# Optimization experiments

Measured on AMD Instinct MI355X. Metric: run time of the kernel, lower is better.

The kernel has to match this reference:

```python
import jax, jax.numpy as jnp
import numpy as np

WINDOW = 64
STRIDE = 4
IMG_H = 512
IMG_W = 512


def _extract_windows(img, W, stride):
    # img: [H, Wd] -> windows [oh*ow, W, W] (row-major over the output grid,
    # matching torch F.unfold ordering)
    H, Wd = img.shape
    oh = (H - W) // stride + 1
    ow = (Wd - W) // stride + 1
    rows = (jnp.arange(oh) * stride)[:, None] + jnp.arange(W)[None, :]   # [oh, W]
    cols = (jnp.arange(ow) * stride)[:, None] + jnp.arange(W)[None, :]   # [ow, W]
    windows = img[rows[:, None, :, None], cols[None, :, None, :]]        # [oh, ow, W, W]
    return windows.reshape(oh * ow, W, W), oh, ow


def setup_inputs() -> dict:
    key = jax.random.key(0)
    X = jax.random.uniform(key, (1, 1, IMG_H, IMG_W), dtype=jnp.float32)
    return {"X": X}


def reference(X):
    W = WINDOW
    stride = STRIDE
    img = X[0, 0]
    windows, oh, ow = _extract_windows(img, W, stride)  # [N, W, W]

    # sizes = 2**arange(log2(W), 1, -1): e.g. W=64 -> [64, 32, 16, 8, 4]
    sizes = (2 ** np.arange(int(np.log2(W)), 1, -1)).astype(np.int64)
    log_sizes = jnp.log(jnp.asarray(sizes, dtype=jnp.float32))  # [S]

    log_db = []
    for s in sizes:
        s = int(s)
        # box partition of each window: [N, W//s, s, W//s, s]
        r = windows.reshape(-1, W // s, s, W // s, s)
        smax = r.max(axis=(2, 4))
        smin = r.min(axis=(2, 4))
        d_b = (smax - smin).sum(axis=(1, 2))  # [N] per-window box-count sum
        log_db.append(jnp.log(d_b))
    log_db = jnp.stack(log_db)  # [S, N]

    # lstsq with a single column (no intercept): slope = <x, y> / <x, x>
    slope = (log_sizes @ log_db) / (log_sizes @ log_sizes)  # [N]
    fd = -slope
    return fd.reshape(1, 1, oh, ow)
```

## Files before the change

### kernel.cpp

```cpp
#include <hip/hip_runtime.h>
#include <math.h>

#define IMG_W 512
#define OW 113
#define N_WIN (113 * 113)
#define LSTRIDE 128

#define OFF4  0
#define OFF8  16384
#define OFF16 32768
#define OFF32 49152
#define OFF64 65536

__device__ __forceinline__ float max4f(float4 v) { return fmaxf(fmaxf(v.x, v.y), fmaxf(v.z, v.w)); }
__device__ __forceinline__ float min4f(float4 v) { return fminf(fminf(v.x, v.y), fminf(v.z, v.w)); }

__global__ __launch_bounds__(256) void fd_pyramid(const float* __restrict__ X,
                                                  float* __restrict__ ws) {
    float* diff4  = ws + OFF4;
    float* diff8  = ws + OFF8;
    float* diff16 = ws + OFF16;
    float* diff32 = ws + OFF32;
    float* diff64 = ws + OFF64;

    const int bi = blockIdx.x >> 4;
    const int bj = blockIdx.x & 15;
    const int r0 = bi * 8, c0 = bj * 8;
    const int t = threadIdx.x;

    __shared__ float tmax[23][24], tmin[23][24];
    __shared__ float p8x[22][24],  p8n[22][24];
    __shared__ float p16x[20][24], p16n[20][24];
    __shared__ float p32x[16][24], p32n[16][24];

    for (int idx = t; idx < 23 * 23; idx += 256) {
        const int lr = idx / 23, lc = idx - lr * 23;
        const int gr = min(r0 + lr, 127);
        const int gc = min(c0 + lc, 127);
        const float* p = X + (gr * 4) * IMG_W + gc * 4;
        float4 a = *(const float4*)(p);
        float4 b = *(const float4*)(p + IMG_W);
        float4 c = *(const float4*)(p + 2 * IMG_W);
        float4 d = *(const float4*)(p + 3 * IMG_W);
        tmax[lr][lc] = fmaxf(fmaxf(max4f(a), max4f(b)), fmaxf(max4f(c), max4f(d)));
        tmin[lr][lc] = fminf(fminf(min4f(a), min4f(b)), fminf(min4f(c), min4f(d)));
    }
    __syncthreads();

    for (int idx = t; idx < 22 * 22; idx += 256) {
        const int lr = idx / 22, lc = idx - lr * 22;
        float x = fmaxf(fmaxf(tmax[lr][lc],     tmax[lr][lc + 1]),
                        fmaxf(tmax[lr + 1][lc], tmax[lr + 1][lc + 1]));
        float n = fminf(fminf(tmin[lr][lc],     tmin[lr][lc + 1]),
                        fminf(tmin[lr + 1][lc], tmin[lr + 1][lc + 1]));
        p8x[lr][lc] = x;
        p8n[lr][lc] = n;
        if (lr < 8 && lc < 8) {
            diff4[(r0 + lr) * LSTRIDE + c0 + lc] = tmax[lr][lc] - tmin[lr][lc];
            diff8[(r0 + lr) * LSTRIDE + c0 + lc] = x - n;
        }
    }
    __syncthreads();

    for (int idx = t; idx < 20 * 20; idx += 256) {
        const int lr = idx / 20, lc = idx - lr * 20;
        float x = fmaxf(fmaxf(p8x[lr][lc],     p8x[lr][lc + 2]),
                        fmaxf(p8x[lr + 2][lc], p8x[lr + 2][lc + 2]));
        float n = fminf(fminf(p8n[lr][lc],     p8n[lr][lc + 2]),
                        fminf(p8n[lr + 2][lc], p8n[lr + 2][lc + 2]));
        p16x[lr][lc] = x;
        p16n[lr][lc] = n;
        if (lr < 8 && lc < 8)
            diff16[(r0 + lr) * LSTRIDE + c0 + lc] = x - n;
    }
    __syncthreads();

    for (int idx = t; idx < 16 * 16; idx += 256) {
        const int lr = idx >> 4, lc = idx & 15;
        float x = fmaxf(fmaxf(p16x[lr][lc],     p16x[lr][lc + 4]),
                        fmaxf(p16x[lr + 4][lc], p16x[lr + 4][lc + 4]));
        float n = fminf(fminf(p16n[lr][lc],     p16n[lr][lc + 4]),
                        fminf(p16n[lr + 4][lc], p16n[lr + 4][lc + 4]));
        p32x[lr][lc] = x;
        p32n[lr][lc] = n;
        if (lr < 8 && lc < 8)
            diff32[(r0 + lr) * LSTRIDE + c0 + lc] = x - n;
    }
    __syncthreads();

    if (t < 64) {
        const int lr = t >> 3, lc = t & 7;
        float x = fmaxf(fmaxf(p32x[lr][lc],     p32x[lr][lc + 8]),
                        fmaxf(p32x[lr + 8][lc], p32x[lr + 8][lc + 8]));
        float n = fminf(fminf(p32n[lr][lc],     p32n[lr][lc + 8]),
                        fminf(p32n[lr + 8][lc], p32n[lr + 8][lc + 8]));
        diff64[(r0 + lr) * LSTRIDE + c0 + lc] = x - n;
    }
}

__global__ __launch_bounds__(256) void fd_final(const float* __restrict__ ws,
                                                float* __restrict__ out) {
    const int w = blockIdx.x * 256 + threadIdx.x;
    if (w >= N_WIN) return;
    const int ti = w / OW;
    const int tj = w - ti * OW;

    const float* diff4  = ws + OFF4;
    const float* diff8  = ws + OFF8;
    const float* diff16 = ws + OFF16;
    const float* diff32 = ws + OFF32;
    const float* diff64 = ws + OFF64;

    float d4 = 0.f;
    #pragma unroll
    for (int a = 0; a < 16; ++a) {
        const float* row = diff4 + (ti + a) * LSTRIDE + tj;
        #pragma unroll
        for (int b = 0; b < 16; ++b) d4 += row[b];
    }
    float d8 = 0.f;
    #pragma unroll
    for (int a = 0; a < 8; ++a) {
        const float* row = diff8 + (ti + 2 * a) * LSTRIDE + tj;
        #pragma unroll
        for (int b = 0; b < 8; ++b) d8 += row[2 * b];
    }
    float d16 = 0.f;
    #pragma unroll
    for (int a = 0; a < 4; ++a) {
        const float* row = diff16 + (ti + 4 * a) * LSTRIDE + tj;
        #pragma unroll
        for (int b = 0; b < 4; ++b) d16 += row[4 * b];
    }
    float d32 = 0.f;
    #pragma unroll
    for (int a = 0; a < 2; ++a) {
        const float* row = diff32 + (ti + 8 * a) * LSTRIDE + tj;
        #pragma unroll
        for (int b = 0; b < 2; ++b) d32 += row[8 * b];
    }
    const float d64 = diff64[ti * LSTRIDE + tj];

    const float LN2 = 0.69314718055994530942f;
    const float num = 6.f * logf(d64) + 5.f * logf(d32) + 4.f * logf(d16)
                    + 3.f * logf(d8)  + 2.f * logf(d4);
    out[w] = -num / (90.0f * LN2);
}

extern "C" void kernel_launch(void* const* d_in, const int* in_sizes, int n_in,
                              void* d_out, int out_size, void* d_ws, size_t ws_size,
                              hipStream_t stream) {
    const float* X = (const float*)d_in[0];
    float* out = (float*)d_out;
    float* ws = (float*)d_ws;
    fd_pyramid<<<256, 256, 0, stream>>>(X, ws);
    fd_final<<<(N_WIN + 255) / 256, 256, 0, stream>>>(ws, out);
}
```

Measured before the change: 61.23 us.

## Fuse pyramid and window-sum kernels into one block-local kernel

Merges the two kernels into one. Each block keeps its per-level max-min differences in shared memory and sums the windows of an 8x8 output tile directly, with four threads per window combined by wavefront shuffles. This removes the global workspace round trip and the second launch. In exchange each block holds more shared memory, and fewer blocks are launched (225 instead of 256).

```diff
diff --git a/kernel.cpp b/kernel.cpp
--- a/kernel.cpp
+++ b/kernel.cpp
@@ -3,47 +3,37 @@
 
 #define IMG_W 512
 #define OW 113
-#define N_WIN (113 * 113)
-#define LSTRIDE 128
-
-#define OFF4  0
-#define OFF8  16384
-#define OFF16 32768
-#define OFF32 49152
-#define OFF64 65536
+#define DS 27
 
 __device__ __forceinline__ float max4f(float4 v) { return fmaxf(fmaxf(v.x, v.y), fmaxf(v.z, v.w)); }
 __device__ __forceinline__ float min4f(float4 v) { return fminf(fminf(v.x, v.y), fminf(v.z, v.w)); }
 
-__global__ __launch_bounds__(256) void fd_pyramid(const float* __restrict__ X,
-                                                  float* __restrict__ ws) {
-    float* diff4  = ws + OFF4;
-    float* diff8  = ws + OFF8;
-    float* diff16 = ws + OFF16;
-    float* diff32 = ws + OFF32;
-    float* diff64 = ws + OFF64;
-
-    const int bi = blockIdx.x >> 4;
-    const int bj = blockIdx.x & 15;
-    const int r0 = bi * 8, c0 = bj * 8;
-    const int t = threadIdx.x;
+__global__ __launch_bounds__(256) void fd_fused(const float* __restrict__ X,
+                                                float* __restrict__ out) {
+    const int bi = blockIdx.x / 15;
+    const int bj = blockIdx.x - bi * 15;
+    const int t  = threadIdx.x;
 
     __shared__ float tmax[23][24], tmin[23][24];
     __shared__ float p8x[22][24],  p8n[22][24];
     __shared__ float p16x[20][24], p16n[20][24];
     __shared__ float p32x[16][24], p32n[16][24];
+    __shared__ float df4[23][DS], df8[22][DS], df16[20][DS], df32[16][DS];
 
     for (int idx = t; idx < 23 * 23; idx += 256) {
         const int lr = idx / 23, lc = idx - lr * 23;
-        const int gr = min(r0 + lr, 127);
-        const int gc = min(c0 + lc, 127);
+        const int gr = min(bi * 8 + lr, 127);
+        const int gc = min(bj * 8 + lc, 127);
         const float* p = X + (gr * 4) * IMG_W + gc * 4;
         float4 a = *(const float4*)(p);
         float4 b = *(const float4*)(p + IMG_W);
         float4 c = *(const float4*)(p + 2 * IMG_W);
         float4 d = *(const float4*)(p + 3 * IMG_W);
-        tmax[lr][lc] = fmaxf(fmaxf(max4f(a), max4f(b)), fmaxf(max4f(c), max4f(d)));
-        tmin[lr][lc] = fminf(fminf(min4f(a), min4f(b)), fminf(min4f(c), min4f(d)));
+        float mx = fmaxf(fmaxf(max4f(a), max4f(b)), fmaxf(max4f(c), max4f(d)));
+        float mn = fminf(fminf(min4f(a), min4f(b)), fminf(min4f(c), min4f(d)));
+        tmax[lr][lc] = mx;
+        tmin[lr][lc] = mn;
+        df4[lr][lc]  = mx - mn;
     }
     __syncthreads();
 
@@ -55,10 +45,7 @@
                         fminf(tmin[lr + 1][lc], tmin[lr + 1][lc + 1]));
         p8x[lr][lc] = x;
         p8n[lr][lc] = n;
-        if (lr < 8 && lc < 8) {
-            diff4[(r0 + lr) * LSTRIDE + c0 + lc] = tmax[lr][lc] - tmin[lr][lc];
-            diff8[(r0 + lr) * LSTRIDE + c0 + lc] = x - n;
-        }
+        df8[lr][lc] = x - n;
     }
     __syncthreads();
 
@@ -70,81 +57,71 @@
                         fminf(p8n[lr + 2][lc], p8n[lr + 2][lc + 2]));
         p16x[lr][lc] = x;
         p16n[lr][lc] = n;
-        if (lr < 8 && lc < 8)
-            diff16[(r0 + lr) * LSTRIDE + c0 + lc] = x - n;
+        df16[lr][lc] = x - n;
     }
     __syncthreads();
 
-    for (int idx = t; idx < 16 * 16; idx += 256) {
-        const int lr = idx >> 4, lc = idx & 15;
+    {
+        const int lr = t >> 4, lc = t & 15;
         float x = fmaxf(fmaxf(p16x[lr][lc],     p16x[lr][lc + 4]),
                         fmaxf(p16x[lr + 4][lc], p16x[lr + 4][lc + 4]));
         float n = fminf(fminf(p16n[lr][lc],     p16n[lr][lc + 4]),
                         fminf(p16n[lr + 4][lc], p16n[lr + 4][lc + 4]));
         p32x[lr][lc] = x;
         p32n[lr][lc] = n;
-        if (lr < 8 && lc < 8)
-            diff32[(r0 + lr) * LSTRIDE + c0 + lc] = x - n;
+        df32[lr][lc] = x - n;
     }
     __syncthreads();
 
-    if (t < 64) {
-        const int lr = t >> 3, lc = t & 7;
-        float x = fmaxf(fmaxf(p32x[lr][lc],     p32x[lr][lc + 8]),
-                        fmaxf(p32x[lr + 8][lc], p32x[lr + 8][lc + 8]));
-        float n = fminf(fminf(p32n[lr][lc],     p32n[lr][lc + 8]),
-                        fminf(p32n[lr + 8][lc], p32n[lr + 8][lc + 8]));
-        diff64[(r0 + lr) * LSTRIDE + c0 + lc] = x - n;
-    }
-}
-
-__global__ __launch_bounds__(256) void fd_final(const float* __restrict__ ws,
-                                                float* __restrict__ out) {
-    const int w = blockIdx.x * 256 + threadIdx.x;
-    if (w >= N_WIN) return;
-    const int ti = w / OW;
-    const int tj = w - ti * OW;
-
-    const float* diff4  = ws + OFF4;
-    const float* diff8  = ws + OFF8;
-    const float* diff16 = ws + OFF16;
-    const float* diff32 = ws + OFF32;
-    const float* diff64 = ws + OFF64;
+    const int q  = t >> 2;
+    const int pp = t & 3;
+    const int wi = q >> 3, wj = q & 7;
 
     float d4 = 0.f;
     #pragma unroll
-    for (int a = 0; a < 16; ++a) {
-        const float* row = diff4 + (ti + a) * LSTRIDE + tj;
+    for (int r = 0; r < 4; ++r) {
+        const float* row = &df4[wi + 4 * pp + r][wj];
         #pragma unroll
         for (int b = 0; b < 16; ++b) d4 += row[b];
     }
     float d8 = 0.f;
     #pragma unroll
-    for (int a = 0; a < 8; ++a) {
-        const float* row = diff8 + (ti + 2 * a) * LSTRIDE + tj;
+    for (int r = 0; r < 2; ++r) {
+        const float* row = &df8[wi + 2 * (2 * pp + r)][wj];
         #pragma unroll
         for (int b = 0; b < 8; ++b) d8 += row[2 * b];
     }
     float d16 = 0.f;
-    #pragma unroll
-    for (int a = 0; a < 4; ++a) {
-        const float* row = diff16 + (ti + 4 * a) * LSTRIDE + tj;
+    {
+        const float* row = &df16[wi + 4 * pp][wj];
         #pragma unroll
         for (int b = 0; b < 4; ++b) d16 += row[4 * b];
     }
-    float d32 = 0.f;
-    #pragma unroll
-    for (int a = 0; a < 2; ++a) {
-        const float* row = diff32 + (ti + 8 * a) * LSTRIDE + tj;
-        #pragma unroll
-        for (int b = 0; b < 2; ++b) d32 += row[8 * b];
+    float d32 = df32[wi + 8 * (pp >> 1)][wj + 8 * (pp & 1)];
+    float d64 = 0.f;
+    if (pp == 0) {
+        float x = fmaxf(fmaxf(p32x[wi][wj],     p32x[wi][wj + 8]),
+                        fmaxf(p32x[wi + 8][wj], p32x[wi + 8][wj + 8]));
+        float n = fminf(fminf(p32n[wi][wj],     p32n[wi][wj + 8]),
+                        fminf(p32n[wi + 8][wj], p32n[wi + 8][wj + 8]));
+        d64 = x - n;
     }
-    const float d64 = diff64[ti * LSTRIDE + tj];
 
-    const float LN2 = 0.69314718055994530942f;
-    const float num = 6.f * logf(d64) + 5.f * logf(d32) + 4.f * logf(d16)
-                    + 3.f * logf(d8)  + 2.f * logf(d4);
-    out[w] = -num / (90.0f * LN2);
+    d4  += __shfl_down(d4,  2, 64);  d4  += __shfl_down(d4,  1, 64);
+    d8  += __shfl_down(d8,  2, 64);  d8  += __shfl_down(d8,  1, 64);
+    d16 += __shfl_down(d16, 2, 64);  d16 += __shfl_down(d16, 1, 64);
+    d32 += __shfl_down(d32, 2, 64);  d32 += __shfl_down(d32, 1, 64);
+
+    if (pp == 0) {
+        const int gwi = bi * 8 + wi;
+        const int gwj = bj * 8 + wj;
+        if (gwi < OW && gwj < OW) {
+            const float LN2 = 0.69314718055994530942f;
+            const float num = 6.f * logf(d64) + 5.f * logf(d32) + 4.f * logf(d16)
+                            + 3.f * logf(d8)  + 2.f * logf(d4);
+            out[gwi * OW + gwj] = -num / (90.0f * LN2);
+        }
+    }
 }
 
 extern "C" void kernel_launch(void* const* d_in, const int* in_sizes, int n_in,
@@ -152,7 +129,5 @@
                               hipStream_t stream) {
     const float* X = (const float*)d_in[0];
     float* out = (float*)d_out;
-    float* ws = (float*)d_ws;
-    fd_pyramid<<<256, 256, 0, stream>>>(X, ws);
-    fd_final<<<(N_WIN + 255) / 256, 256, 0, stream>>>(ws, out);
+    fd_fused<<<15 * 15, 256, 0, stream>>>(X, out);
 }
```

After: 58.49 us. 4.5% less time.
